# Kernel tuning notes

Measured on AMD Instinct MI355X. Metric: run time of the kernel, lower is better.

The kernel has to match this reference:

```python
import jax, jax.numpy as jnp
import numpy as np

S, B, HID = 2048, 1, 2048
NH, HD = 16, 128  # heads, head_dim (kv_channels); NH*HD == HID
EPS = 1e-5


def setup_inputs() -> dict:
    key = jax.random.key(0)
    ks = jax.random.split(key, 5)
    sc_h = 1.0 / np.sqrt(HID)
    return {
        "hidden_states": jax.random.normal(ks[0], (S, B, HID), jnp.float32),
        "ln_weight": jnp.ones((HID,), jnp.float32),
        "ln_bias": jnp.zeros((HID,), jnp.float32),
        "qkv_weight": jax.random.normal(ks[1], (3 * HID, HID), jnp.float32) * sc_h,
        "qkv_bias": jax.random.normal(ks[2], (3 * HID,), jnp.float32) * 0.02,
        "proj_weight": jax.random.normal(ks[3], (HID, HID), jnp.float32) * sc_h,
        "proj_bias": jax.random.normal(ks[4], (HID,), jnp.float32) * 0.02,
    }


def reference(hidden_states, ln_weight, ln_bias, qkv_weight, qkv_bias, proj_weight, proj_bias):
    s, b, hid = hidden_states.shape
    # LayerNormLinear: LN over last dim, then fused QKV projection
    mu = jnp.mean(hidden_states, axis=-1, keepdims=True)
    var = jnp.mean(jnp.square(hidden_states - mu), axis=-1, keepdims=True)
    ln_x = (hidden_states - mu) * jax.lax.rsqrt(var + EPS) * ln_weight + ln_bias
    mixed = jnp.einsum('sbh,oh->sbo', ln_x, qkv_weight) + qkv_bias  # [S,B,3*HID]
    # fuse_qkv_params=False -> non-interleaved: reshape to [S,B,3*NH,HD], split on dim -2
    mixed = mixed.reshape(s, b, 3 * NH, HD)
    q, k, v = jnp.split(mixed, 3, axis=2)  # each [S,B,NH,HD]
    # scaled dot-product attention with causal mask
    scale = 1.0 / np.sqrt(HD)
    scores = jnp.einsum('sbhd,tbhd->bhst', q, k) * scale  # [B,NH,S,S]
    causal = jnp.tril(jnp.ones((s, s), bool))
    scores = jnp.where(causal, scores, -jnp.inf)
    probs = jax.nn.softmax(scores, axis=-1)
    ctx = jnp.einsum('bhst,tbhd->sbhd', probs, v).reshape(s, b, hid)
    # output projection
    out = jnp.einsum('sbh,oh->sbo', ctx, proj_weight) + proj_bias
    return out
```

## Files before the change

### kernel.cpp

```cpp
#include <hip/hip_runtime.h>
#include <stdint.h>

#define S_LEN 2048
#define HID   2048
#define NHEAD 16
#define HDIM  128
#define LDQK  4096

typedef unsigned short ushort_t;
using bf16x8 = __attribute__((ext_vector_type(8))) short;
using f32x4  = __attribute__((ext_vector_type(4))) float;

__device__ __forceinline__ float bf2f(ushort_t u) {
  union { uint32_t i; float f; } v; v.i = ((uint32_t)u) << 16; return v.f;
}
__device__ __forceinline__ ushort_t f2bf(float f) {
  union { float f; uint32_t i; } v; v.f = f;
  uint32_t r = v.i + 0x7fffu + ((v.i >> 16) & 1u);
  return (ushort_t)(r >> 16);
}
__device__ __forceinline__ void store_val(ushort_t* C, size_t idx, float v) { C[idx] = f2bf(v); }
__device__ __forceinline__ void store_val(float* C, size_t idx, float v) { C[idx] = v; }

__device__ __forceinline__ bf16x8 load8(const ushort_t* p) { return *(const bf16x8*)p; }
__device__ __forceinline__ bf16x8 load8(const float* p) {
  float4 a = *(const float4*)p, b = *(const float4*)(p + 4);
  ushort_t o[8] = { f2bf(a.x), f2bf(a.y), f2bf(a.z), f2bf(a.w),
                    f2bf(b.x), f2bf(b.y), f2bf(b.z), f2bf(b.w) };
  return *(const bf16x8*)o;
}

__device__ __forceinline__ void gl_lds16(const ushort_t* g, short* l) {
  __builtin_amdgcn_global_load_lds((const __attribute__((address_space(1))) void*)g,
                                   (__attribute__((address_space(3))) void*)l, 16, 0, 0);
}

__global__ __launch_bounds__(256) void cvt_f32_bf16(const float* __restrict__ src,
                                                    ushort_t* __restrict__ dst, int n8) {
  int i = blockIdx.x * 256 + threadIdx.x;
  if (i >= n8) return;
  float4 a = ((const float4*)src)[i * 2], b = ((const float4*)src)[i * 2 + 1];
  ushort_t o[8] = { f2bf(a.x), f2bf(a.y), f2bf(a.z), f2bf(a.w),
                    f2bf(b.x), f2bf(b.y), f2bf(b.z), f2bf(b.w) };
  ((uint4*)dst)[i] = *(const uint4*)o;
}

__global__ __launch_bounds__(256) void ln_kernel(const float* __restrict__ x,
                                                 const float* __restrict__ w,
                                                 const float* __restrict__ b,
                                                 ushort_t* __restrict__ y) {
  const int row = blockIdx.x;
  const int t = threadIdx.x;
  const float4* xr = (const float4*)(x + (size_t)row * HID);
  float4 v0 = xr[t], v1 = xr[t + 256];
  float s  = v0.x + v0.y + v0.z + v0.w + v1.x + v1.y + v1.z + v1.w;
  float ss = v0.x*v0.x + v0.y*v0.y + v0.z*v0.z + v0.w*v0.w
           + v1.x*v1.x + v1.y*v1.y + v1.z*v1.z + v1.w*v1.w;
#pragma unroll
  for (int off = 32; off > 0; off >>= 1) { s += __shfl_xor(s, off, 64); ss += __shfl_xor(ss, off, 64); }
  __shared__ float red[8];
  const int wv = t >> 6;
  if ((t & 63) == 0) { red[wv * 2] = s; red[wv * 2 + 1] = ss; }
  __syncthreads();
  s  = red[0] + red[2] + red[4] + red[6];
  ss = red[1] + red[3] + red[5] + red[7];
  const float mu   = s * (1.f / HID);
  const float var  = ss * (1.f / HID) - mu * mu;
  const float rstd = rsqrtf(var + 1e-5f);
  const float4* wr = (const float4*)w;
  const float4* br = (const float4*)b;
  float4 w0 = wr[t], w1 = wr[t + 256];
  float4 b0 = br[t], b1 = br[t + 256];
  ushort_t* yr = y + (size_t)row * HID;
  ushort_t o0[4] = { f2bf((v0.x - mu) * rstd * w0.x + b0.x), f2bf((v0.y - mu) * rstd * w0.y + b0.y),
                     f2bf((v0.z - mu) * rstd * w0.z + b0.z), f2bf((v0.w - mu) * rstd * w0.w + b0.w) };
  ushort_t o1[4] = { f2bf((v1.x - mu) * rstd * w1.x + b1.x), f2bf((v1.y - mu) * rstd * w1.y + b1.y),
                     f2bf((v1.z - mu) * rstd * w1.z + b1.z), f2bf((v1.w - mu) * rstd * w1.w + b1.w) };
  *(uint2*)(&yr[4 * t])         = *(const uint2*)o0;
  *(uint2*)(&yr[4 * (t + 256)]) = *(const uint2*)o1;
}

template <int MT, bool SPLIT, typename OUT_T>
__global__ __launch_bounds__(256, 3) void gemm_lds(const ushort_t* __restrict__ A,
                                                   const ushort_t* __restrict__ B,
                                                   const float* __restrict__ bias,
                                                   OUT_T* __restrict__ C,
                                                   ushort_t* __restrict__ VTg,
                                                   int M, int N, int K, int ldc) {
  constexpr int MI = MT / 32;
  __shared__ __align__(16) short As[2][MT * 32];
  __shared__ __align__(16) short Bs[2][128 * 32];
  const int mb = blockIdx.x * MT, nb = blockIdx.y * 128;
  const int t = threadIdx.x, wave = t >> 6, lane = t & 63;
  const int wm = (wave >> 1) * (MT / 2), wn = (wave & 1) * 64;
  const int lrow = lane & 15, quad = lane >> 4;
  const int srow = lane >> 2, scol = (lane & 3) * 8;
  const f32x4 vzero = {0.f, 0.f, 0.f, 0.f};

  f32x4 acc[MI][4];
#pragma unroll
  for (int i = 0; i < MI; i++)
#pragma unroll
    for (int j = 0; j < 4; j++) acc[i][j] = vzero;

  auto stage = [&](int k0, int buf) {
#pragma unroll
    for (int kb = 0; kb < MT / 64; kb++) {
      const int c = wave * (MT / 64) + kb;
      gl_lds16(&A[(size_t)(mb + c * 16 + srow) * K + k0 + scol], &As[buf][c * 512]);
    }
#pragma unroll
    for (int kb = 0; kb < 2; kb++) {
      const int c = wave * 2 + kb;
      gl_lds16(&B[(size_t)(nb + c * 16 + srow) * K + k0 + scol], &Bs[buf][c * 512]);
    }
  };

  stage(0, 0);
  int cur = 0;
  for (int k0 = 0; k0 < K; k0 += 32) {
    __syncthreads();
    if (k0 + 32 < K) stage(k0 + 32, cur ^ 1);
    bf16x8 af[MI], bfg[4];
#pragma unroll
    for (int mi = 0; mi < MI; mi++) af[mi] = *(const bf16x8*)(&As[cur][(wm + mi * 16 + lrow) * 32 + quad * 8]);
#pragma unroll
    for (int ni = 0; ni < 4; ni++) bfg[ni] = *(const bf16x8*)(&Bs[cur][(wn + ni * 16 + lrow) * 32 + quad * 8]);
#pragma unroll
    for (int mi = 0; mi < MI; mi++)
#pragma unroll
      for (int ni = 0; ni < 4; ni++)
        acc[mi][ni] = __builtin_amdgcn_mfma_f32_16x16x32_bf16(af[mi], bfg[ni], acc[mi][ni], 0, 0, 0);
    cur ^= 1;
  }

#pragma unroll
  for (int mi = 0; mi < MI; mi++)
#pragma unroll
    for (int ni = 0; ni < 4; ni++) {
      const int col = nb + wn + ni * 16 + lrow;
      const float bv = bias[col];
      const int row0 = mb + wm + mi * 16 + quad * 4;
      if (SPLIT && col >= 4096) {
        ushort_t o4[4];
#pragma unroll
        for (int r = 0; r < 4; r++) o4[r] = f2bf(acc[mi][ni][r] + bv);
        *(uint2*)(&VTg[(size_t)(col - 4096) * S_LEN + row0]) = *(const uint2*)o4;
      } else {
#pragma unroll
        for (int r = 0; r < 4; r++)
          store_val(C, (size_t)(row0 + r) * ldc + col, acc[mi][ni][r] + bv);
      }
    }
}

template <bool SPLIT, typename OUT_T, typename BT>
__global__ __launch_bounds__(256, 3) void gemm_bt(const ushort_t* __restrict__ A,
                                                  const BT* __restrict__ B,
                                                  const float* __restrict__ bias,
                                                  OUT_T* __restrict__ C,
                                                  ushort_t* __restrict__ VTg,
                                                  int M, int N, int K, int ldc) {
  __shared__ __align__(16) short As[128 * 40];
  __shared__ __align__(16) short Bs[128 * 40];
  const int mb = blockIdx.x * 128, nb = blockIdx.y * 128;
  const int t = threadIdx.x, wave = t >> 6, lane = t & 63;
  const int wm = (wave >> 1) * 64, wn = (wave & 1) * 64;
  const int lrow = lane & 15, quad = lane >> 4;
  const f32x4 vzero = {0.f, 0.f, 0.f, 0.f};
  f32x4 acc[4][4];
#pragma unroll
  for (int i = 0; i < 4; i++)
#pragma unroll
    for (int j = 0; j < 4; j++) acc[i][j] = vzero;
  for (int k0 = 0; k0 < K; k0 += 32) {
    __syncthreads();
#pragma unroll
    for (int i = 0; i < 2; i++) {
      int c = t + 256 * i;
      int r = c >> 2, kc = (c & 3) * 8;
      *(bf16x8*)(&As[r * 40 + kc]) = load8(&A[(size_t)(mb + r) * K + k0 + kc]);
      *(bf16x8*)(&Bs[r * 40 + kc]) = load8(&B[(size_t)(nb + r) * K + k0 + kc]);
    }
    __syncthreads();
    bf16x8 af[4], bfg[4];
#pragma unroll
    for (int mi = 0; mi < 4; mi++) af[mi] = *(const bf16x8*)(&As[(wm + mi * 16 + lrow) * 40 + quad * 8]);
#pragma unroll
    for (int ni = 0; ni < 4; ni++) bfg[ni] = *(const bf16x8*)(&Bs[(wn + ni * 16 + lrow) * 40 + quad * 8]);
#pragma unroll
    for (int mi = 0; mi < 4; mi++)
#pragma unroll
      for (int ni = 0; ni < 4; ni++)
        acc[mi][ni] = __builtin_amdgcn_mfma_f32_16x16x32_bf16(af[mi], bfg[ni], acc[mi][ni], 0, 0, 0);
  }
#pragma unroll
  for (int mi = 0; mi < 4; mi++)
#pragma unroll
    for (int ni = 0; ni < 4; ni++) {
      const int col = nb + wn + ni * 16 + lrow;
      const float bv = bias[col];
      const int row0 = mb + wm + mi * 16 + quad * 4;
      if (SPLIT && col >= 4096) {
        ushort_t o4[4];
#pragma unroll
        for (int r = 0; r < 4; r++) o4[r] = f2bf(acc[mi][ni][r] + bv);
        *(uint2*)(&VTg[(size_t)(col - 4096) * S_LEN + row0]) = *(const uint2*)o4;
      } else {
#pragma unroll
        for (int r = 0; r < 4; r++)
          store_val(C, (size_t)(row0 + r) * ldc + col, acc[mi][ni][r] + bv);
      }
    }
}

__global__ __launch_bounds__(256, 2) void attn_kernel(const ushort_t* __restrict__ mixedQK,
                                                      const ushort_t* __restrict__ vtg,
                                                      ushort_t* __restrict__ ctx) {
  const int b = blockIdx.x;
  const int h = b & 15;
  const int p = b >> 4;
  const int t = threadIdx.x;
  const int wave = t >> 6, lane = t & 63;
  const int lrow = lane & 15, quad = lane >> 4;
  const float scale = 0.08838834764831845f;
  const float SHIFT = 8.0f;

  __shared__ __align__(16) short Ks[2][64 * 128];
  __shared__ __align__(16) short VTs[2][128 * 64];
  __shared__ __align__(16) short Ps[4][16 * 72];

  const int krow_off = wave * 4 + (lane >> 4);
  const int kgrp = (lane & 15) ^ krow_off;
  const int vrow_off = wave * 8 + (lane >> 3);
  const int vgrp = (lane & 7) ^ (lane >> 3);
  const ushort_t* Kbase = mixedQK + 2048 + h * HDIM;
  const ushort_t* Vbase = vtg + (size_t)h * HDIM * S_LEN;

  const f32x4 vzero = {0.f, 0.f, 0.f, 0.f};
  int cur = 0;

#pragma unroll
  for (int i = 0; i < 4; i++)
    gl_lds16(Kbase + (size_t)(i * 16 + krow_off) * LDQK + kgrp * 8,
             &Ks[cur][(i * 256 + wave * 64) * 8]);
#pragma unroll
  for (int i = 0; i < 4; i++)
    gl_lds16(Vbase + (size_t)(i * 32 + vrow_off) * S_LEN + vgrp * 8,
             &VTs[cur][(i * 256 + wave * 64) * 8]);

  for (int item = 0; item < 2; ++item) {
    const int qblk = item ? (31 - p) : p;
    const int ntiles = qblk + 1;
    const int q0 = qblk * 64 + wave * 16;

    bf16x8 qf[4];
    {
      const ushort_t* Qb = mixedQK + (size_t)(q0 + lrow) * LDQK + h * HDIM;
#pragma unroll
      for (int c = 0; c < 4; c++) qf[c] = *(const bf16x8*)(Qb + c * 32 + quad * 8);
    }

    float lsum[4] = {0.f, 0.f, 0.f, 0.f};
    f32x4 acc[8];
#pragma unroll
    for (int d = 0; d < 8; d++) acc[d] = vzero;

    for (int tk = 0; tk < ntiles; ++tk) {
      const int kv0 = tk * 64;
      __syncthreads();

      const int nv0 = (tk + 1 < ntiles) ? (tk + 1) * 64 : (item == 0 ? 0 : -1);
      if (nv0 >= 0) {
#pragma unroll
        for (int i = 0; i < 4; i++)
          gl_lds16(Kbase + (size_t)(nv0 + i * 16 + krow_off) * LDQK + kgrp * 8,
                   &Ks[cur ^ 1][(i * 256 + wave * 64) * 8]);
#pragma unroll
        for (int i = 0; i < 4; i++)
          gl_lds16(Vbase + (size_t)(i * 32 + vrow_off) * S_LEN + nv0 + vgrp * 8,
                   &VTs[cur ^ 1][(i * 256 + wave * 64) * 8]);
      }

      const short* Kc = Ks[cur];
      const short* Vc = VTs[cur];

      f32x4 sc[4];
#pragma unroll
      for (int ni = 0; ni < 4; ni++) sc[ni] = vzero;
#pragma unroll
      for (int ni = 0; ni < 4; ni++)
#pragma unroll
        for (int c = 0; c < 4; c++) {
          bf16x8 kf = *(const bf16x8*)(&Kc[(((ni * 16 + lrow) << 4) + ((c * 4 + quad) ^ lrow)) * 8]);
          sc[ni] = __builtin_amdgcn_mfma_f32_16x16x32_bf16(qf[c], kf, sc[ni], 0, 0, 0);
        }

      short* P = &Ps[wave][0];
#pragma unroll
      for (int r = 0; r < 4; r++) {
        const int row = q0 + quad * 4 + r;
#pragma unroll
        for (int ni = 0; ni < 4; ni++) {
          const int col = kv0 + ni * 16 + lrow;
          float pe = (col > row) ? 0.f : __expf(sc[ni][r] * scale - SHIFT);
          lsum[r] += pe;
          P[(quad * 4 + r) * 72 + ni * 16 + lrow] = (short)f2bf(pe);
        }
      }

      bf16x8 pf[2];
#pragma unroll
      for (int c = 0; c < 2; c++) pf[c] = *(const bf16x8*)(&P[lrow * 72 + c * 32 + quad * 8]);
#pragma unroll
      for (int d = 0; d < 8; d++)
#pragma unroll
        for (int c = 0; c < 2; c++) {
          bf16x8 vf = *(const bf16x8*)(&Vc[(((d * 16 + lrow) << 3) + ((c * 4 + quad) ^ (lrow & 7))) * 8]);
          acc[d] = __builtin_amdgcn_mfma_f32_16x16x32_bf16(pf[c], vf, acc[d], 0, 0, 0);
        }

      cur ^= 1;
    }

    float inv_l[4];
#pragma unroll
    for (int r = 0; r < 4; r++) {
      float l = lsum[r];
#pragma unroll
      for (int off = 1; off < 16; off <<= 1) l += __shfl_xor(l, off, 16);
      inv_l[r] = 1.f / l;
    }
#pragma unroll
    for (int d = 0; d < 8; d++)
#pragma unroll
      for (int r = 0; r < 4; r++) {
        const int row = q0 + quad * 4 + r;
        ctx[(size_t)row * HID + h * HDIM + d * 16 + lrow] = f2bf(acc[d][r] * inv_l[r]);
      }
  }
}

extern "C" void kernel_launch(void* const* d_in, const int* in_sizes, int n_in,
                              void* d_out, int out_size, void* d_ws, size_t ws_size,
                              hipStream_t stream) {
  const float* hidden = (const float*)d_in[0];
  const float* lnw    = (const float*)d_in[1];
  const float* lnb    = (const float*)d_in[2];
  const float* qkvw   = (const float*)d_in[3];
  const float* qkvb   = (const float*)d_in[4];
  const float* projw  = (const float*)d_in[5];
  const float* projb  = (const float*)d_in[6];
  float* out = (float*)d_out;

  char* ws = (char*)d_ws;
  ushort_t* ln_x    = (ushort_t*)ws;
  ushort_t* mixedQK = (ushort_t*)(ws + ((size_t)8 << 20));
  ushort_t* vtg     = (ushort_t*)(ws + ((size_t)24 << 20));
  ushort_t* qkvw_bf = (ushort_t*)(ws + ((size_t)32 << 20));
  ushort_t* projw_bf= (ushort_t*)(ws + ((size_t)56 << 20));
  ushort_t* ctxb    = ln_x;
  const bool big = ws_size >= ((size_t)64 << 20);

  ln_kernel<<<S_LEN, 256, 0, stream>>>(hidden, lnw, lnb, ln_x);
  if (big) {
    cvt_f32_bf16<<<6144, 256, 0, stream>>>(qkvw, qkvw_bf, 3 * HID * HID / 8);
    cvt_f32_bf16<<<2048, 256, 0, stream>>>(projw, projw_bf, HID * HID / 8);
    gemm_lds<128, true, ushort_t><<<dim3(16, 48), 256, 0, stream>>>(
        ln_x, qkvw_bf, qkvb, mixedQK, vtg, S_LEN, 3 * HID, HID, LDQK);
  } else {
    gemm_bt<true, ushort_t, float><<<dim3(16, 48), 256, 0, stream>>>(
        ln_x, qkvw, qkvb, mixedQK, vtg, S_LEN, 3 * HID, HID, LDQK);
  }
  attn_kernel<<<256, 256, 0, stream>>>(mixedQK, vtg, ctxb);
  if (big) {
    gemm_lds<64, false, float><<<dim3(32, 16), 256, 0, stream>>>(
        ctxb, projw_bf, projb, out, nullptr, S_LEN, HID, HID, HID);
  } else {
    gemm_bt<false, float, float><<<dim3(16, 16), 256, 0, stream>>>(
        ctxb, projw, projb, out, nullptr, S_LEN, HID, HID, HID);
  }
}
```

Measured before the change: 273.7 us.

## Merge weight conversions, swizzle GEMM LDS, and share KV tiles across paired query blocks

Three independent changes. The two weight-conversion launches become one kernel. The GEMM gains a templated K-tile depth with an XOR-swizzled LDS layout to cut bank conflicts, and the output projection uses BK=64. The attention kernel now processes its two paired query blocks together over one shared KV stream, so K/V tiles are loaded into LDS once instead of being streamed twice. This roughly doubles accumulator registers in attention, which may hurt occupancy or cause spills.

```diff
diff --git a/kernel.cpp b/kernel.cpp
--- a/kernel.cpp
+++ b/kernel.cpp
@@ -35,14 +35,19 @@
                                    (__attribute__((address_space(3))) void*)l, 16, 0, 0);
 }
 
-__global__ __launch_bounds__(256) void cvt_f32_bf16(const float* __restrict__ src,
-                                                    ushort_t* __restrict__ dst, int n8) {
+__global__ __launch_bounds__(256) void cvt2_f32_bf16(const float* __restrict__ s1,
+                                                     ushort_t* __restrict__ d1, int n1,
+                                                     const float* __restrict__ s2,
+                                                     ushort_t* __restrict__ d2, int n2) {
   int i = blockIdx.x * 256 + threadIdx.x;
-  if (i >= n8) return;
-  float4 a = ((const float4*)src)[i * 2], b = ((const float4*)src)[i * 2 + 1];
+  const float* s; ushort_t* d; int j;
+  if (i < n1) { s = s1; d = d1; j = i; }
+  else if (i < n1 + n2) { s = s2; d = d2; j = i - n1; }
+  else return;
+  float4 a = ((const float4*)s)[j * 2], b = ((const float4*)s)[j * 2 + 1];
   ushort_t o[8] = { f2bf(a.x), f2bf(a.y), f2bf(a.z), f2bf(a.w),
                     f2bf(b.x), f2bf(b.y), f2bf(b.z), f2bf(b.w) };
-  ((uint4*)dst)[i] = *(const uint4*)o;
+  ((uint4*)d)[j] = *(const uint4*)o;
 }
 
 __global__ __launch_bounds__(256) void ln_kernel(const float* __restrict__ x,
@@ -80,7 +85,7 @@
   *(uint2*)(&yr[4 * (t + 256)]) = *(const uint2*)o1;
 }
 
-template <int MT, bool SPLIT, typename OUT_T>
+template <int MT, int BK, bool SPLIT, typename OUT_T>
 __global__ __launch_bounds__(256, 3) void gemm_lds(const ushort_t* __restrict__ A,
                                                    const ushort_t* __restrict__ B,
                                                    const float* __restrict__ bias,
@@ -88,13 +93,19 @@
                                                    ushort_t* __restrict__ VTg,
                                                    int M, int N, int K, int ldc) {
   constexpr int MI = MT / 32;
-  __shared__ __align__(16) short As[2][MT * 32];
-  __shared__ __align__(16) short Bs[2][128 * 32];
+  constexpr int G  = BK / 8;
+  constexpr int ACH = MT * BK / 512;
+  constexpr int BCH = 128 * BK / 512;
+  __shared__ __align__(16) short As[2][MT * BK];
+  __shared__ __align__(16) short Bs[2][128 * BK];
   const int mb = blockIdx.x * MT, nb = blockIdx.y * 128;
   const int t = threadIdx.x, wave = t >> 6, lane = t & 63;
   const int wm = (wave >> 1) * (MT / 2), wn = (wave & 1) * 64;
   const int lrow = lane & 15, quad = lane >> 4;
-  const int srow = lane >> 2, scol = (lane & 3) * 8;
+  const int srow = (BK == 32) ? (lane >> 2) : (lane >> 3);
+  const int sgrp = (BK == 32) ? ((lane & 3) ^ ((lane >> 3) & 3))
+                              : ((lane & 7) ^ ((lane >> 3) & 7));
+  const int rhash = (BK == 32) ? ((lrow >> 1) & 3) : (lrow & 7);
   const f32x4 vzero = {0.f, 0.f, 0.f, 0.f};
 
   f32x4 acc[MI][4];
@@ -105,32 +116,37 @@
 
   auto stage = [&](int k0, int buf) {
 #pragma unroll
-    for (int kb = 0; kb < MT / 64; kb++) {
-      const int c = wave * (MT / 64) + kb;
-      gl_lds16(&A[(size_t)(mb + c * 16 + srow) * K + k0 + scol], &As[buf][c * 512]);
-    }
-#pragma unroll
-    for (int kb = 0; kb < 2; kb++) {
-      const int c = wave * 2 + kb;
-      gl_lds16(&B[(size_t)(nb + c * 16 + srow) * K + k0 + scol], &Bs[buf][c * 512]);
+    for (int kb = 0; kb < ACH / 4; kb++) {
+      const int c = wave * (ACH / 4) + kb;
+      gl_lds16(&A[(size_t)(mb + c * (64 / G) + srow) * K + k0 + sgrp * 8], &As[buf][c * 512]);
+    }
+#pragma unroll
+    for (int kb = 0; kb < BCH / 4; kb++) {
+      const int c = wave * (BCH / 4) + kb;
+      gl_lds16(&B[(size_t)(nb + c * (64 / G) + srow) * K + k0 + sgrp * 8], &Bs[buf][c * 512]);
     }
   };
 
   stage(0, 0);
   int cur = 0;
-  for (int k0 = 0; k0 < K; k0 += 32) {
+  for (int k0 = 0; k0 < K; k0 += BK) {
     __syncthreads();
-    if (k0 + 32 < K) stage(k0 + 32, cur ^ 1);
-    bf16x8 af[MI], bfg[4];
-#pragma unroll
-    for (int mi = 0; mi < MI; mi++) af[mi] = *(const bf16x8*)(&As[cur][(wm + mi * 16 + lrow) * 32 + quad * 8]);
-#pragma unroll
-    for (int ni = 0; ni < 4; ni++) bfg[ni] = *(const bf16x8*)(&Bs[cur][(wn + ni * 16 + lrow) * 32 + quad * 8]);
-#pragma unroll
-    for (int mi = 0; mi < MI; mi++)
+    if (k0 + BK < K) stage(k0 + BK, cur ^ 1);
+#pragma unroll
+    for (int ks = 0; ks < BK / 32; ks++) {
+      bf16x8 af[MI], bfg[4];
+#pragma unroll
+      for (int mi = 0; mi < MI; mi++)
+        af[mi] = *(const bf16x8*)(&As[cur][(wm + mi * 16 + lrow) * BK + ((ks * 4 + quad) ^ rhash) * 8]);
 #pragma unroll
       for (int ni = 0; ni < 4; ni++)
-        acc[mi][ni] = __builtin_amdgcn_mfma_f32_16x16x32_bf16(af[mi], bfg[ni], acc[mi][ni], 0, 0, 0);
+        bfg[ni] = *(const bf16x8*)(&Bs[cur][(wn + ni * 16 + lrow) * BK + ((ks * 4 + quad) ^ rhash) * 8]);
+#pragma unroll
+      for (int mi = 0; mi < MI; mi++)
+#pragma unroll
+        for (int ni = 0; ni < 4; ni++)
+          acc[mi][ni] = __builtin_amdgcn_mfma_f32_16x16x32_bf16(af[mi], bfg[ni], acc[mi][ni], 0, 0, 0);
+    }
     cur ^= 1;
   }
 
@@ -214,17 +230,60 @@
     }
 }
 
+static __device__ __forceinline__ void attn_tile(const short* __restrict__ Kc,
+                                                 const short* __restrict__ Vc,
+                                                 short* __restrict__ P,
+                                                 const bf16x8 (&qf)[4], f32x4 (&acc)[8],
+                                                 float (&ls)[4], int q0, int kv0,
+                                                 int lrow, int quad) {
+  const float scale = 0.08838834764831845f;
+  const float SHIFT = 8.0f;
+  const f32x4 vzero = {0.f, 0.f, 0.f, 0.f};
+  f32x4 sc[4];
+#pragma unroll
+  for (int ni = 0; ni < 4; ni++) sc[ni] = vzero;
+#pragma unroll
+  for (int ni = 0; ni < 4; ni++)
+#pragma unroll
+    for (int c = 0; c < 4; c++) {
+      bf16x8 kf = *(const bf16x8*)(&Kc[(((ni * 16 + lrow) << 4) + ((c * 4 + quad) ^ lrow)) * 8]);
+      sc[ni] = __builtin_amdgcn_mfma_f32_16x16x32_bf16(qf[c], kf, sc[ni], 0, 0, 0);
+    }
+#pragma unroll
+  for (int r = 0; r < 4; r++) {
+    const int row = q0 + quad * 4 + r;
+#pragma unroll
+    for (int ni = 0; ni < 4; ni++) {
+      const int col = kv0 + ni * 16 + lrow;
+      float pe = (col > row) ? 0.f : __expf(sc[ni][r] * scale - SHIFT);
+      ls[r] += pe;
+      P[(quad * 4 + r) * 72 + ni * 16 + lrow] = (short)f2bf(pe);
+    }
+  }
+  bf16x8 pf[2];
+#pragma unroll
+  for (int c = 0; c < 2; c++) pf[c] = *(const bf16x8*)(&P[lrow * 72 + c * 32 + quad * 8]);
+#pragma unroll
+  for (int d = 0; d < 8; d++)
+#pragma unroll
+    for (int c = 0; c < 2; c++) {
+      bf16x8 vf = *(const bf16x8*)(&Vc[(((d * 16 + lrow) << 3) + ((c * 4 + quad) ^ (lrow & 7))) * 8]);
+      acc[d] = __builtin_amdgcn_mfma_f32_16x16x32_bf16(pf[c], vf, acc[d], 0, 0, 0);
+    }
+}
+
 __global__ __launch_bounds__(256, 2) void attn_kernel(const ushort_t* __restrict__ mixedQK,
                                                       const ushort_t* __restrict__ vtg,
                                                       ushort_t* __restrict__ ctx) {
   const int b = blockIdx.x;
   const int h = b & 15;
   const int p = b >> 4;
+  const int qA = p, qB = 31 - p;
+  const int ntB = qB + 1;
   const int t = threadIdx.x;
   const int wave = t >> 6, lane = t & 63;
   const int lrow = lane & 15, quad = lane >> 4;
-  const float scale = 0.08838834764831845f;
-  const float SHIFT = 8.0f;
+  const int q0A = qA * 64 + wave * 16, q0B = qB * 64 + wave * 16;
 
   __shared__ __align__(16) short Ks[2][64 * 128];
   __shared__ __align__(16) short VTs[2][128 * 64];
@@ -237,108 +296,60 @@
   const ushort_t* Kbase = mixedQK + 2048 + h * HDIM;
   const ushort_t* Vbase = vtg + (size_t)h * HDIM * S_LEN;
 
+  auto stage = [&](int kv0, int buf) {
+#pragma unroll
+    for (int i = 0; i < 4; i++)
+      gl_lds16(Kbase + (size_t)(kv0 + i * 16 + krow_off) * LDQK + kgrp * 8,
+               &Ks[buf][(i * 256 + wave * 64) * 8]);
+#pragma unroll
+    for (int i = 0; i < 4; i++)
+      gl_lds16(Vbase + (size_t)(i * 32 + vrow_off) * S_LEN + kv0 + vgrp * 8,
+               &VTs[buf][(i * 256 + wave * 64) * 8]);
+  };
+
+  bf16x8 qfA[4], qfB[4];
+  {
+    const ushort_t* QbA = mixedQK + (size_t)(q0A + lrow) * LDQK + h * HDIM;
+    const ushort_t* QbB = mixedQK + (size_t)(q0B + lrow) * LDQK + h * HDIM;
+#pragma unroll
+    for (int c = 0; c < 4; c++) { qfA[c] = *(const bf16x8*)(QbA + c * 32 + quad * 8);
+                                  qfB[c] = *(const bf16x8*)(QbB + c * 32 + quad * 8); }
+  }
+
   const f32x4 vzero = {0.f, 0.f, 0.f, 0.f};
+  float lsA[4] = {0,0,0,0}, lsB[4] = {0,0,0,0};
+  f32x4 accA[8], accB[8];
+#pragma unroll
+  for (int d = 0; d < 8; d++) { accA[d] = vzero; accB[d] = vzero; }
+
+  stage(0, 0);
   int cur = 0;
-
-#pragma unroll
-  for (int i = 0; i < 4; i++)
-    gl_lds16(Kbase + (size_t)(i * 16 + krow_off) * LDQK + kgrp * 8,
-             &Ks[cur][(i * 256 + wave * 64) * 8]);
-#pragma unroll
-  for (int i = 0; i < 4; i++)
-    gl_lds16(Vbase + (size_t)(i * 32 + vrow_off) * S_LEN + vgrp * 8,
-             &VTs[cur][(i * 256 + wave * 64) * 8]);
-
-  for (int item = 0; item < 2; ++item) {
-    const int qblk = item ? (31 - p) : p;
-    const int ntiles = qblk + 1;
-    const int q0 = qblk * 64 + wave * 16;
-
-    bf16x8 qf[4];
-    {
-      const ushort_t* Qb = mixedQK + (size_t)(q0 + lrow) * LDQK + h * HDIM;
-#pragma unroll
-      for (int c = 0; c < 4; c++) qf[c] = *(const bf16x8*)(Qb + c * 32 + quad * 8);
-    }
-
-    float lsum[4] = {0.f, 0.f, 0.f, 0.f};
-    f32x4 acc[8];
-#pragma unroll
-    for (int d = 0; d < 8; d++) acc[d] = vzero;
-
-    for (int tk = 0; tk < ntiles; ++tk) {
-      const int kv0 = tk * 64;
-      __syncthreads();
-
-      const int nv0 = (tk + 1 < ntiles) ? (tk + 1) * 64 : (item == 0 ? 0 : -1);
-      if (nv0 >= 0) {
-#pragma unroll
-        for (int i = 0; i < 4; i++)
-          gl_lds16(Kbase + (size_t)(nv0 + i * 16 + krow_off) * LDQK + kgrp * 8,
-                   &Ks[cur ^ 1][(i * 256 + wave * 64) * 8]);
-#pragma unroll
-        for (int i = 0; i < 4; i++)
-          gl_lds16(Vbase + (size_t)(i * 32 + vrow_off) * S_LEN + nv0 + vgrp * 8,
-                   &VTs[cur ^ 1][(i * 256 + wave * 64) * 8]);
-      }
-
-      const short* Kc = Ks[cur];
-      const short* Vc = VTs[cur];
-
-      f32x4 sc[4];
-#pragma unroll
-      for (int ni = 0; ni < 4; ni++) sc[ni] = vzero;
-#pragma unroll
-      for (int ni = 0; ni < 4; ni++)
-#pragma unroll
-        for (int c = 0; c < 4; c++) {
-          bf16x8 kf = *(const bf16x8*)(&Kc[(((ni * 16 + lrow) << 4) + ((c * 4 + quad) ^ lrow)) * 8]);
-          sc[ni] = __builtin_amdgcn_mfma_f32_16x16x32_bf16(qf[c], kf, sc[ni], 0, 0, 0);
-        }
-
-      short* P = &Ps[wave][0];
-#pragma unroll
-      for (int r = 0; r < 4; r++) {
-        const int row = q0 + quad * 4 + r;
-#pragma unroll
-        for (int ni = 0; ni < 4; ni++) {
-          const int col = kv0 + ni * 16 + lrow;
-          float pe = (col > row) ? 0.f : __expf(sc[ni][r] * scale - SHIFT);
-          lsum[r] += pe;
-          P[(quad * 4 + r) * 72 + ni * 16 + lrow] = (short)f2bf(pe);
-        }
-      }
-
-      bf16x8 pf[2];
-#pragma unroll
-      for (int c = 0; c < 2; c++) pf[c] = *(const bf16x8*)(&P[lrow * 72 + c * 32 + quad * 8]);
-#pragma unroll
-      for (int d = 0; d < 8; d++)
-#pragma unroll
-        for (int c = 0; c < 2; c++) {
-          bf16x8 vf = *(const bf16x8*)(&Vc[(((d * 16 + lrow) << 3) + ((c * 4 + quad) ^ (lrow & 7))) * 8]);
-          acc[d] = __builtin_amdgcn_mfma_f32_16x16x32_bf16(pf[c], vf, acc[d], 0, 0, 0);
-        }
-
-      cur ^= 1;
-    }
-
-    float inv_l[4];
+  for (int tk = 0; tk < ntB; ++tk) {
+    const int kv0 = tk * 64;
+    __syncthreads();
+    if (tk + 1 < ntB) stage((tk + 1) * 64, cur ^ 1);
+    const short* Kc = Ks[cur];
+    const short* Vc = VTs[cur];
+    short* P = &Ps[wave][0];
+    attn_tile(Kc, Vc, P, qfB, accB, lsB, q0B, kv0, lrow, quad);
+    if (tk <= p) attn_tile(Kc, Vc, P, qfA, accA, lsA, q0A, kv0, lrow, quad);
+    cur ^= 1;
+  }
+
+#pragma unroll
+  for (int r = 0; r < 4; r++) {
+    float la = lsA[r], lb = lsB[r];
+#pragma unroll
+    for (int off = 1; off < 16; off <<= 1) { la += __shfl_xor(la, off, 16); lb += __shfl_xor(lb, off, 16); }
+    lsA[r] = 1.f / la; lsB[r] = 1.f / lb;
+  }
+#pragma unroll
+  for (int d = 0; d < 8; d++)
 #pragma unroll
     for (int r = 0; r < 4; r++) {
-      float l = lsum[r];
-#pragma unroll
-      for (int off = 1; off < 16; off <<= 1) l += __shfl_xor(l, off, 16);
-      inv_l[r] = 1.f / l;
-    }
-#pragma unroll
-    for (int d = 0; d < 8; d++)
-#pragma unroll
-      for (int r = 0; r < 4; r++) {
-        const int row = q0 + quad * 4 + r;
-        ctx[(size_t)row * HID + h * HDIM + d * 16 + lrow] = f2bf(acc[d][r] * inv_l[r]);
-      }
-  }
+      ctx[(size_t)(q0A + quad * 4 + r) * HID + h * HDIM + d * 16 + lrow] = f2bf(accA[d][r] * lsA[r]);
+      ctx[(size_t)(q0B + quad * 4 + r) * HID + h * HDIM + d * 16 + lrow] = f2bf(accB[d][r] * lsB[r]);
+    }
 }
 
 extern "C" void kernel_launch(void* const* d_in, const int* in_sizes, int n_in,
@@ -364,9 +375,9 @@
 
   ln_kernel<<<S_LEN, 256, 0, stream>>>(hidden, lnw, lnb, ln_x);
   if (big) {
-    cvt_f32_bf16<<<6144, 256, 0, stream>>>(qkvw, qkvw_bf, 3 * HID * HID / 8);
-    cvt_f32_bf16<<<2048, 256, 0, stream>>>(projw, projw_bf, HID * HID / 8);
-    gemm_lds<128, true, ushort_t><<<dim3(16, 48), 256, 0, stream>>>(
+    const int n1 = 3 * HID * HID / 8, n2 = HID * HID / 8;
+    cvt2_f32_bf16<<<(n1 + n2 + 255) / 256, 256, 0, stream>>>(qkvw, qkvw_bf, n1, projw, projw_bf, n2);
+    gemm_lds<128, 32, true, ushort_t><<<dim3(16, 48), 256, 0, stream>>>(
         ln_x, qkvw_bf, qkvb, mixedQK, vtg, S_LEN, 3 * HID, HID, LDQK);
   } else {
     gemm_bt<true, ushort_t, float><<<dim3(16, 48), 256, 0, stream>>>(
@@ -374,7 +385,7 @@
   }
   attn_kernel<<<256, 256, 0, stream>>>(mixedQK, vtg, ctxb);
   if (big) {
-    gemm_lds<64, false, float><<<dim3(32, 16), 256, 0, stream>>>(
+    gemm_lds<64, 64, false, float><<<dim3(32, 16), 256, 0, stream>>>(
         ctxb, projw_bf, projb, out, nullptr, S_LEN, HID, HID, HID);
   } else {
     gemm_bt<false, float, float><<<dim3(16, 16), 256, 0, stream>>>(
```

After: 393.5 us. 1.44x slower.
